# Kernel tuning notes

Hardware: AMD Instinct MI355X
Metric: run time of the kernel (lower is better)

Reference implementation:

```python
import jax, jax.numpy as jnp
import numpy as np
from jax import lax

B, DIM, H, W = 32, 256, 56, 56
HID = 4 * DIM
EPS = 1e-6


def setup_inputs() -> dict:
    key = jax.random.key(0)
    ks = jax.random.split(key, 8)
    x = jax.random.normal(ks[0], (B, DIM, H, W), dtype=jnp.float32)
    # depthwise conv: OIHW with feature_group_count=DIM -> [DIM, 1, 7, 7]
    conv_w = jax.random.normal(ks[1], (DIM, 1, 7, 7), dtype=jnp.float32) * 0.05
    conv_b = jax.random.normal(ks[2], (DIM,), dtype=jnp.float32) * 0.01
    ln_g = jnp.ones((DIM,), dtype=jnp.float32)
    ln_b = jnp.zeros((DIM,), dtype=jnp.float32)
    w1 = jax.random.normal(ks[3], (DIM, HID), dtype=jnp.float32) * (1.0 / np.sqrt(DIM))
    b1 = jax.random.normal(ks[4], (HID,), dtype=jnp.float32) * 0.01
    w2 = jax.random.normal(ks[5], (HID, DIM), dtype=jnp.float32) * (1.0 / np.sqrt(HID))
    b2 = jax.random.normal(ks[6], (DIM,), dtype=jnp.float32) * 0.01
    return {"x": x, "conv_w": conv_w, "conv_b": conv_b, "ln_g": ln_g,
            "ln_b": ln_b, "w1": w1, "b1": b1, "w2": w2, "b2": b2}


def reference(x, conv_w, conv_b, ln_g, ln_b, w1, b1, w2, b2):
    dim = x.shape[1]
    # 7x7 depthwise conv, stride 1, padding 3 (NCHW)
    y = lax.conv_general_dilated(
        x, conv_w, window_strides=(1, 1), padding=((3, 3), (3, 3)),
        dimension_numbers=("NCHW", "OIHW", "NCHW"), feature_group_count=dim)
    y = y + conv_b[None, :, None, None]
    # permute to NHWC
    y = jnp.transpose(y, (0, 2, 3, 1))  # [B, H, W, C]
    # LayerNorm over channel (last) dim, eps=1e-6, affine
    mu = jnp.mean(y, axis=-1, keepdims=True)
    var = jnp.mean(jnp.square(y - mu), axis=-1, keepdims=True)
    y = (y - mu) * lax.rsqrt(var + EPS) * ln_g + ln_b
    # MLP: Linear -> exact GELU -> Linear
    h = jax.nn.gelu(jnp.einsum("bhwc,cf->bhwf", y, w1) + b1, approximate=False)
    y = jnp.einsum("bhwf,fc->bhwc", h, w2) + b2
    # permute back to NCHW; stochastic depth is identity at eval time
    return jnp.transpose(y, (0, 3, 1, 2))
```

## Files before the change

kernel.cpp:

```cpp
#include <hip/hip_runtime.h>
#include <math.h>

#define CDIM 256
#define HW 3136
#define HID 1024

typedef __attribute__((ext_vector_type(4))) float f32x4;
typedef __attribute__((ext_vector_type(8))) short bf16x8;
typedef __attribute__((ext_vector_type(4))) short bf16x4;

__device__ __forceinline__ unsigned short f2bf(float f){
  unsigned int u = __float_as_uint(f);
  u += 0x7FFFu + ((u >> 16) & 1u);
  return (unsigned short)(u >> 16);
}

__device__ __forceinline__ void load_lds16(const void* g, void* l){
  __builtin_amdgcn_global_load_lds(
      (const __attribute__((address_space(1))) unsigned int*)g,
      (__attribute__((address_space(3))) unsigned int*)l, 16, 0, 0);
}

__global__ __launch_bounds__(256) void prep_kernel(
    const float* __restrict__ w1, const float* __restrict__ w2,
    unsigned short* __restrict__ w1t, unsigned short* __restrict__ w2t){
  int i = blockIdx.x * 256 + threadIdx.x;
  if (i < 262144){
    int f = i >> 8, c = i & 255;
    w1t[i] = f2bf(w1[c * 1024 + f]);
  } else {
    int j = i - 262144;
    int c = j >> 10, f = j & 1023;
    w2t[j] = f2bf(w2[f * 256 + c]);
  }
}

__global__ __launch_bounds__(256) void conv_kernel(
    const float* __restrict__ x, const float* __restrict__ cw,
    const float* __restrict__ cb, float* __restrict__ t0){
  int bc = blockIdx.x;
  int c = bc & 255;
  int t = threadIdx.x;
  int h = t >> 2;
  int w0 = (t & 3) * 14;
  float wt[49];
  #pragma unroll
  for (int k = 0; k < 49; ++k) wt[k] = cw[c * 49 + k];
  float bias = cb[c];
  if (h >= 56) return;
  const float* xp = x + (long)bc * HW;
  float acc[14];
  #pragma unroll
  for (int ww = 0; ww < 14; ++ww) acc[ww] = bias;
  #pragma unroll
  for (int i = 0; i < 7; ++i){
    int hh = h - 3 + i;
    if (hh >= 0 && hh < 56){
      float seg[20];
      #pragma unroll
      for (int k = 0; k < 20; ++k){
        int col = w0 - 3 + k;
        seg[k] = (col >= 0 && col < 56) ? xp[hh * 56 + col] : 0.0f;
      }
      #pragma unroll
      for (int j = 0; j < 7; ++j){
        #pragma unroll
        for (int ww = 0; ww < 14; ++ww)
          acc[ww] = fmaf(seg[ww + j], wt[i * 7 + j], acc[ww]);
      }
    }
  }
  float* op = t0 + (long)bc * HW + h * 56 + w0;
  #pragma unroll
  for (int ww = 0; ww < 14; ++ww) op[ww] = acc[ww];
}

__global__ __launch_bounds__(256) void ln_kernel(
    const float* __restrict__ t0, const float* __restrict__ lng,
    const float* __restrict__ lnb, unsigned short* __restrict__ y){
  __shared__ float tile[256 * 68];
  __shared__ float part_s[256];
  __shared__ float part_q[256];
  __shared__ float lg_s[256];
  __shared__ float lb_s[256];
  const int t = threadIdx.x, wv = t >> 6, lane = t & 63;
  const int pos0 = blockIdx.x * 64;
  const int b = pos0 / HW;
  const int hw0 = pos0 - b * HW;
  const float* tp = t0 + (long)b * CDIM * HW + hw0;

  lg_s[t] = lng[t];
  lb_s[t] = lnb[t];

  float s = 0.f, q = 0.f;
  #pragma unroll 8
  for (int i = 0; i < 64; ++i){
    int c = wv * 64 + i;
    float v = tp[c * HW + lane];
    tile[c * 68 + lane] = v;
    s += v; q = fmaf(v, v, q);
  }
  part_s[wv * 64 + lane] = s;
  part_q[wv * 64 + lane] = q;
  __syncthreads();

  const int p = t >> 2, c0 = (t & 3) * 64;
  float S = part_s[p] + part_s[64 + p] + part_s[128 + p] + part_s[192 + p];
  float Q = part_q[p] + part_q[64 + p] + part_q[128 + p] + part_q[192 + p];
  float mu = S * (1.0f / 256.0f);
  float var = Q * (1.0f / 256.0f) - mu * mu;
  float rs = rsqrtf(var + 1e-6f);

  unsigned short* yp = y + (long)(pos0 + p) * 256 + c0;
  #pragma unroll
  for (int j = 0; j < 8; ++j){
    bf16x8 o;
    #pragma unroll
    for (int k = 0; k < 8; ++k){
      int c = c0 + j * 8 + k;
      float v = tile[c * 68 + p];
      o[k] = (short)f2bf((v - mu) * rs * lg_s[c] + lb_s[c]);
    }
    *(bf16x8*)(yp + j * 8) = o;
  }
}

#define LDS_H0 33792
#define MLP_LDS (33792 + 18432)
#define YA_ROW(m) ((((m) >> 1) * 1056) + (((m) & 1) * 512))

__global__ __launch_bounds__(256, 3) void mlp_kernel(
    const unsigned short* __restrict__ y, const unsigned short* __restrict__ w1t,
    const unsigned short* __restrict__ w2t, const float* __restrict__ b1,
    const float* __restrict__ b2, float* __restrict__ out){
  __shared__ __align__(16) unsigned char smem[MLP_LDS];
  const int t = threadIdx.x;
  const int wv = t >> 6, lane = t & 63;
  const int lr = lane & 15, lq = lane >> 4;
  const int blk = blockIdx.x;

  {
    const unsigned char* ybase = (const unsigned char*)(y + (long)blk * 64 * 256);
    #pragma unroll
    for (int r = 0; r < 8; ++r){
      int g = wv * 8 + r;
      load_lds16(ybase + g * 1024 + lane * 16, smem + g * 1056);
    }
  }

  f32x4 acc2[4][4];
  #pragma unroll
  for (int a = 0; a < 4; ++a)
    #pragma unroll
    for (int bb = 0; bb < 4; ++bb) acc2[a][bb] = (f32x4){0.f, 0.f, 0.f, 0.f};

  __syncthreads();

  for (int ch = 0; ch < 16; ++ch){
    unsigned char* Hbuf = smem + LDS_H0 + (ch & 1) * 9216;

    const unsigned short* w1p = w1t + (((long)ch * 64 + wv * 16 + lr) << 8);
    bf16x8 wf[8];
    #pragma unroll
    for (int ks = 0; ks < 8; ++ks)
      wf[ks] = *(const bf16x8*)(w1p + ks * 32 + lq * 8);

    f32x4 acc1[4];
    #pragma unroll
    for (int mt = 0; mt < 4; ++mt) acc1[mt] = (f32x4){0.f, 0.f, 0.f, 0.f};
    #pragma unroll
    for (int ks = 0; ks < 8; ++ks){
      bf16x8 yf[4];
      #pragma unroll
      for (int mt = 0; mt < 4; ++mt)
        yf[mt] = *(const bf16x8*)(smem + YA_ROW(mt * 16 + lr) + ks * 64 + lq * 16);
      #pragma unroll
      for (int mt = 0; mt < 4; ++mt)
        acc1[mt] = __builtin_amdgcn_mfma_f32_16x16x32_bf16(wf[ks], yf[mt], acc1[mt], 0, 0, 0);
    }

    bf16x8 w2f[2][4];
    #pragma unroll
    for (int ks2 = 0; ks2 < 2; ++ks2)
      #pragma unroll
      for (int ct = 0; ct < 4; ++ct)
        w2f[ks2][ct] = *(const bf16x8*)(w2t + (long)(wv * 64 + ct * 16 + lr) * 1024
                                        + ch * 64 + ks2 * 32 + lq * 8);

    {
      f32x4 bv = *(const f32x4*)(b1 + ch * 64 + wv * 16 + lq * 4);
      #pragma unroll
      for (int mt = 0; mt < 4; ++mt){
        bf16x4 hv;
        #pragma unroll
        for (int r = 0; r < 4; ++r){
          float pv = acc1[mt][r] + bv[r];
          float gl = 0.5f * pv * (1.0f + erff(pv * 0.70710678118654752f));
          hv[r] = (short)f2bf(gl);
        }
        *(bf16x4*)(Hbuf + (mt * 16 + lr) * 144 + wv * 32 + lq * 8) = hv;
      }
    }
    __syncthreads();

    #pragma unroll
    for (int ks2 = 0; ks2 < 2; ++ks2){
      bf16x8 hf[4];
      #pragma unroll
      for (int mt = 0; mt < 4; ++mt)
        hf[mt] = *(const bf16x8*)(Hbuf + (mt * 16 + lr) * 144 + ks2 * 64 + lq * 16);
      #pragma unroll
      for (int ct = 0; ct < 4; ++ct)
        #pragma unroll
        for (int mt = 0; mt < 4; ++mt)
          acc2[ct][mt] = __builtin_amdgcn_mfma_f32_16x16x32_bf16(w2f[ks2][ct], hf[mt], acc2[ct][mt], 0, 0, 0);
    }
  }

  #pragma unroll
  for (int ct = 0; ct < 4; ++ct){
    int cb = wv * 64 + ct * 16 + lq * 4;
    f32x4 b2v = *(const f32x4*)(b2 + cb);
    #pragma unroll
    for (int mt = 0; mt < 4; ++mt){
      int m = mt * 16 + lr;
      unsigned pos = (unsigned)(blk * 64 + m);
      unsigned bimg = pos / 3136u;
      unsigned hw = pos - bimg * 3136u;
      float* op = out + ((long)bimg * 256 + cb) * 3136 + hw;
      #pragma unroll
      for (int r = 0; r < 4; ++r)
        op[r * 3136] = acc2[ct][mt][r] + b2v[r];
    }
  }
}

extern "C" void kernel_launch(void* const* d_in, const int* in_sizes, int n_in,
                              void* d_out, int out_size, void* d_ws, size_t ws_size,
                              hipStream_t stream){
  const float* x  = (const float*)d_in[0];
  const float* cw = (const float*)d_in[1];
  const float* cb = (const float*)d_in[2];
  const float* lg = (const float*)d_in[3];
  const float* lb = (const float*)d_in[4];
  const float* w1 = (const float*)d_in[5];
  const float* b1 = (const float*)d_in[6];
  const float* w2 = (const float*)d_in[7];
  const float* b2 = (const float*)d_in[8];
  float* out = (float*)d_out;

  unsigned short* y   = (unsigned short*)d_ws;
  unsigned short* w1t = (unsigned short*)((char*)d_ws + 51380224);
  unsigned short* w2t = (unsigned short*)((char*)d_ws + 51904512);

  hipLaunchKernelGGL(prep_kernel, dim3(2048), dim3(256), 0, stream, w1, w2, w1t, w2t);
  hipLaunchKernelGGL(conv_kernel, dim3(8192), dim3(256), 0, stream, x, cw, cb, out);
  hipLaunchKernelGGL(ln_kernel,  dim3(1568), dim3(256), 0, stream, out, lg, lb, y);
  hipLaunchKernelGGL(mlp_kernel, dim3(1568), dim3(256), 0, stream, y, w1t, w2t, b1, b2, out);
}
```

Baseline: 580.6 us.

## Fuse depthwise conv with LayerNorm per image row; use tanh-approx GELU

Merges the depthwise 7x7 conv and the channel LayerNorm into one kernel. Each block now handles one (batch, row) pair with one thread per channel, keeps the 56-wide row of conv outputs in registers, and transposes through shared memory for the per-pixel statistics. This drops the fp32 intermediate write and re-read through global memory and removes one launch. The exact erf GELU is also replaced by a tanh-style sigmoid approximation built on exp2 and rcp, which cuts transcendental cost but changes the numerics slightly. The fused kernel uses more registers per thread and reads input rows with strided per-channel loads.

```diff
diff --git a/kernel.cpp b/kernel.cpp
--- a/kernel.cpp
+++ b/kernel.cpp
@@ -35,93 +35,99 @@
   }
 }
 
-__global__ __launch_bounds__(256) void conv_kernel(
+__global__ __launch_bounds__(256) void convln_kernel(
     const float* __restrict__ x, const float* __restrict__ cw,
-    const float* __restrict__ cb, float* __restrict__ t0){
-  int bc = blockIdx.x;
-  int c = bc & 255;
-  int t = threadIdx.x;
-  int h = t >> 2;
-  int w0 = (t & 3) * 14;
-  float wt[49];
-  #pragma unroll
-  for (int k = 0; k < 49; ++k) wt[k] = cw[c * 49 + k];
-  float bias = cb[c];
-  if (h >= 56) return;
-  const float* xp = x + (long)bc * HW;
-  float acc[14];
-  #pragma unroll
-  for (int ww = 0; ww < 14; ++ww) acc[ww] = bias;
-  #pragma unroll
+    const float* __restrict__ cb, const float* __restrict__ lng,
+    const float* __restrict__ lnb, unsigned short* __restrict__ y){
+  __shared__ float tile[256 * 61];
+  __shared__ float part_s[4][64];
+  __shared__ float part_q[4][64];
+  __shared__ float lg_s[256];
+  __shared__ float lb_s[256];
+
+  const int t = threadIdx.x;
+  const int blk = blockIdx.x;
+  const int b = blk / 56;
+  const int h = blk - b * 56;
+  const int c = t;
+
+  lg_s[t] = lng[t];
+  lb_s[t] = lnb[t];
+
+  float acc[56];
+  {
+    float bias = cb[c];
+    #pragma unroll
+    for (int w = 0; w < 56; ++w) acc[w] = bias;
+  }
+
+  const float* xim = x + (long)(b * 256 + c) * HW;
+  const float* cwc = cw + c * 49;
   for (int i = 0; i < 7; ++i){
     int hh = h - 3 + i;
     if (hh >= 0 && hh < 56){
-      float seg[20];
-      #pragma unroll
-      for (int k = 0; k < 20; ++k){
-        int col = w0 - 3 + k;
-        seg[k] = (col >= 0 && col < 56) ? xp[hh * 56 + col] : 0.0f;
-      }
+      float seg[62];
+      seg[0] = seg[1] = seg[2] = 0.f;
+      seg[59] = seg[60] = seg[61] = 0.f;
+      const float* xrow = xim + hh * 56;
+      #pragma unroll
+      for (int w4 = 0; w4 < 14; ++w4){
+        f32x4 v = *(const f32x4*)(xrow + w4 * 4);
+        seg[3 + w4 * 4 + 0] = v[0];
+        seg[3 + w4 * 4 + 1] = v[1];
+        seg[3 + w4 * 4 + 2] = v[2];
+        seg[3 + w4 * 4 + 3] = v[3];
+      }
+      float wt7[7];
+      #pragma unroll
+      for (int j = 0; j < 7; ++j) wt7[j] = cwc[i * 7 + j];
       #pragma unroll
       for (int j = 0; j < 7; ++j){
+        float wj = wt7[j];
         #pragma unroll
-        for (int ww = 0; ww < 14; ++ww)
-          acc[ww] = fmaf(seg[ww + j], wt[i * 7 + j], acc[ww]);
-      }
-    }
-  }
-  float* op = t0 + (long)bc * HW + h * 56 + w0;
+        for (int w = 0; w < 56; ++w)
+          acc[w] = fmaf(seg[w + j], wj, acc[w]);
+      }
+    }
+  }
+
   #pragma unroll
-  for (int ww = 0; ww < 14; ++ww) op[ww] = acc[ww];
-}
-
-__global__ __launch_bounds__(256) void ln_kernel(
-    const float* __restrict__ t0, const float* __restrict__ lng,
-    const float* __restrict__ lnb, unsigned short* __restrict__ y){
-  __shared__ float tile[256 * 68];
-  __shared__ float part_s[256];
-  __shared__ float part_q[256];
-  __shared__ float lg_s[256];
-  __shared__ float lb_s[256];
-  const int t = threadIdx.x, wv = t >> 6, lane = t & 63;
-  const int pos0 = blockIdx.x * 64;
-  const int b = pos0 / HW;
-  const int hw0 = pos0 - b * HW;
-  const float* tp = t0 + (long)b * CDIM * HW + hw0;
-
-  lg_s[t] = lng[t];
-  lb_s[t] = lnb[t];
-
-  float s = 0.f, q = 0.f;
-  #pragma unroll 8
-  for (int i = 0; i < 64; ++i){
-    int c = wv * 64 + i;
-    float v = tp[c * HW + lane];
-    tile[c * 68 + lane] = v;
-    s += v; q = fmaf(v, v, q);
-  }
-  part_s[wv * 64 + lane] = s;
-  part_q[wv * 64 + lane] = q;
+  for (int p = 0; p < 56; ++p) tile[c * 61 + p] = acc[p];
   __syncthreads();
 
-  const int p = t >> 2, c0 = (t & 3) * 64;
-  float S = part_s[p] + part_s[64 + p] + part_s[128 + p] + part_s[192 + p];
-  float Q = part_q[p] + part_q[64 + p] + part_q[128 + p] + part_q[192 + p];
-  float mu = S * (1.0f / 256.0f);
-  float var = Q * (1.0f / 256.0f) - mu * mu;
-  float rs = rsqrtf(var + 1e-6f);
-
-  unsigned short* yp = y + (long)(pos0 + p) * 256 + c0;
-  #pragma unroll
-  for (int j = 0; j < 8; ++j){
-    bf16x8 o;
-    #pragma unroll
-    for (int k = 0; k < 8; ++k){
-      int c = c0 + j * 8 + k;
-      float v = tile[c * 68 + p];
-      o[k] = (short)f2bf((v - mu) * rs * lg_s[c] + lb_s[c]);
-    }
-    *(bf16x8*)(yp + j * 8) = o;
+  {
+    int p = t & 63; if (p > 55) p = 55;
+    const int q = t >> 6;
+    float s = 0.f, qq = 0.f;
+    #pragma unroll 8
+    for (int j = 0; j < 64; ++j){
+      float v = tile[(q * 64 + j) * 61 + p];
+      s += v; qq = fmaf(v, v, qq);
+    }
+    part_s[q][p] = s;
+    part_q[q][p] = qq;
+  }
+  __syncthreads();
+
+  if (t < 224){
+    const int p = t >> 2, c0 = (t & 3) * 64;
+    float S = part_s[0][p] + part_s[1][p] + part_s[2][p] + part_s[3][p];
+    float Q = part_q[0][p] + part_q[1][p] + part_q[2][p] + part_q[3][p];
+    float mu = S * (1.0f / 256.0f);
+    float var = Q * (1.0f / 256.0f) - mu * mu;
+    float rs = rsqrtf(var + 1e-6f);
+    unsigned short* yp = y + ((long)blk * 56 + p) * 256 + c0;
+    #pragma unroll
+    for (int j = 0; j < 8; ++j){
+      bf16x8 o;
+      #pragma unroll
+      for (int k = 0; k < 8; ++k){
+        int cc = c0 + j * 8 + k;
+        float v = tile[cc * 61 + p];
+        o[k] = (short)f2bf((v - mu) * rs * lg_s[cc] + lb_s[cc]);
+      }
+      *(bf16x8*)(yp + j * 8) = o;
+    }
   }
 }
 
@@ -195,7 +201,10 @@
         #pragma unroll
         for (int r = 0; r < 4; ++r){
           float pv = acc1[mt][r] + bv[r];
-          float gl = 0.5f * pv * (1.0f + erff(pv * 0.70710678118654752f));
+          float p2 = pv * pv;
+          float u  = pv * fmaf(0.044715f, p2, 1.0f);
+          float e  = __builtin_amdgcn_exp2f(-2.3022083f * u);
+          float gl = pv * __builtin_amdgcn_rcpf(1.0f + e);
           hv[r] = (short)f2bf(gl);
         }
         *(bf16x4*)(Hbuf + (mt * 16 + lr) * 144 + wv * 32 + lq * 8) = hv;
@@ -253,8 +262,7 @@
   unsigned short* w1t = (unsigned short*)((char*)d_ws + 51380224);
   unsigned short* w2t = (unsigned short*)((char*)d_ws + 51904512);
 
-  hipLaunchKernelGGL(prep_kernel, dim3(2048), dim3(256), 0, stream, w1, w2, w1t, w2t);
-  hipLaunchKernelGGL(conv_kernel, dim3(8192), dim3(256), 0, stream, x, cw, cb, out);
-  hipLaunchKernelGGL(ln_kernel,  dim3(1568), dim3(256), 0, stream, out, lg, lb, y);
-  hipLaunchKernelGGL(mlp_kernel, dim3(1568), dim3(256), 0, stream, y, w1t, w2t, b1, b2, out);
-}
+  hipLaunchKernelGGL(prep_kernel,   dim3(2048), dim3(256), 0, stream, w1, w2, w1t, w2t);
+  hipLaunchKernelGGL(convln_kernel, dim3(1792), dim3(256), 0, stream, x, cw, cb, lg, lb, y);
+  hipLaunchKernelGGL(mlp_kernel,    dim3(1568), dim3(256), 0, stream, y, w1t, w2t, b1, b2, out);
+}
```

New measurement: 528.8 us. 1.1x faster.
